# Kernel optimization log

Measured on AMD Instinct MI355X. Metric: run time of the kernel, lower is better.

Reference implementation:

```python
import jax, jax.numpy as jnp
import numpy as np

N_NODES = 50000
N_EDGES = 1600000
D_V, D_E, D_ATTN = 256, 128, 128


def setup_inputs() -> dict:
    key = jax.random.key(0)
    ks = jax.random.split(key, 10)
    scale = 0.05
    nodes = jax.random.normal(ks[0], (N_NODES, D_V), dtype=jnp.float32)
    edges = jax.random.normal(ks[1], (N_EDGES, D_E), dtype=jnp.float32)
    edge_index = jax.random.randint(ks[2], (2, N_EDGES), 0, N_NODES, dtype=jnp.int64 if jax.config.jax_enable_x64 else jnp.int32)
    Wq = jax.random.normal(ks[3], (D_ATTN, D_V), dtype=jnp.float32) * scale
    bq = jnp.zeros((D_ATTN,), dtype=jnp.float32)
    Wk = jax.random.normal(ks[4], (D_ATTN, D_V), dtype=jnp.float32) * scale
    bk = jnp.zeros((D_ATTN,), dtype=jnp.float32)
    Wv = jax.random.normal(ks[5], (D_ATTN, D_E), dtype=jnp.float32) * scale
    bv = jnp.zeros((D_ATTN,), dtype=jnp.float32)
    return {"nodes": nodes, "edges": edges, "edge_index": edge_index,
            "Wq": Wq, "bq": bq, "Wk": Wk, "bk": bk, "Wv": Wv, "bv": bv}


def reference(nodes, edges, edge_index, Wq, bq, Wk, bk, Wv, bv):
    # nodes: [N, d_v], edges: [E, d_e], edge_index: [2, E] (s=sender, r=receiver)
    s, r = edge_index[0], edge_index[1]
    lrelu = jax.nn.leaky_relu  # default negative_slope=0.01, matches torch F.leaky_relu
    q = lrelu(nodes @ Wq.T + bq)      # [N, d_attn]
    k = lrelu(nodes[s] @ Wk.T + bk)   # [E, d_attn]  (key of sender node per edge)
    v = lrelu(edges @ Wv.T + bv)      # [E, d_attn]
    d = q.shape[-1]
    # Per-edge logit = <q[r[e]], k[e]> / sqrt(d).  Masked dense softmax over the
    # [N, E] score matrix with mask (r[e]==i) is exactly a segment softmax by receiver.
    logits = jnp.sum(q[r] * k, axis=-1) / jnp.sqrt(jnp.asarray(d, q.dtype))  # [E]
    N = nodes.shape[0]
    m = jax.ops.segment_max(logits, r, num_segments=N)          # [N]
    p = jnp.exp(logits - m[r])                                  # [E]
    denom = jax.ops.segment_sum(p, r, num_segments=N)           # [N]
    attn = p / denom[r]                                         # [E]
    out = jax.ops.segment_sum(attn[:, None] * v, r, num_segments=N)  # [N, d_attn]
    return out
```

## Files before the change

### kernel.cpp

```cpp
#include <hip/hip_runtime.h>
#include <hip/hip_bf16.h>
#include <cstdint>

#define NN 50000
#define NE 1600000
#define DV 256
#define DA 128

using floatx4 = __attribute__((ext_vector_type(4))) float;
using shortx8 = __attribute__((ext_vector_type(8))) short;

__device__ __forceinline__ unsigned short f2bf(float f) {
    union { float f; uint32_t u; } v; v.f = f;
    uint32_t u = v.u;
    uint32_t r = (u + 0x7FFFu + ((u >> 16) & 1u)) >> 16;
    return (unsigned short)r;
}
__device__ __forceinline__ float bflo(uint32_t u) {
    union { uint32_t u; float f; } v; v.u = u << 16; return v.f;
}
__device__ __forceinline__ float bfhi(uint32_t u) {
    union { uint32_t u; float f; } v; v.u = u & 0xFFFF0000u; return v.f;
}

__global__ void init_zero(float4* __restrict__ out, float4* __restrict__ denom,
                          float4* __restrict__ cnt) {
    const float4 z = make_float4(0.f, 0.f, 0.f, 0.f);
    int i = blockIdx.x * blockDim.x + threadIdx.x;
    const int stride = gridDim.x * blockDim.x;
    for (int j = i; j < NN * 128 / 4; j += stride) out[j] = z;
    if (i < NN / 4) { denom[i] = z; cnt[i] = z; }
}

__global__ void cast_w_kernel(const float* __restrict__ wq, const float* __restrict__ wk,
                              const float* __restrict__ wv, unsigned short* __restrict__ out) {
    int i = blockIdx.x * blockDim.x + threadIdx.x;
    if (i < 32768)       out[i] = f2bf(wq[i]);
    else if (i < 65536)  out[i] = f2bf(wk[i - 32768]);
    else if (i < 81920)  out[i] = f2bf(wv[i - 65536]);
}

__global__ void hist_kernel(const int* __restrict__ ridx, int* __restrict__ cnt) {
    int e = blockIdx.x * blockDim.x + threadIdx.x;
    if (e < NE) atomicAdd(&cnt[ridx[e]], 1);
}

__global__ __launch_bounds__(1024)
void scan_kernel(const int* __restrict__ cnt, int* __restrict__ offs) {
    __shared__ int part[1024];
    const int tid = threadIdx.x;
    const int PER = (NN + 1023) / 1024;
    int base = tid * PER;
    int s = 0;
    for (int i = 0; i < PER; ++i) { int idx = base + i; if (idx < NN) s += cnt[idx]; }
    part[tid] = s;
    __syncthreads();
    for (int off = 1; off < 1024; off <<= 1) {
        int v = (tid >= off) ? part[tid - off] : 0;
        __syncthreads();
        part[tid] += v;
        __syncthreads();
    }
    int excl = (tid == 0) ? 0 : part[tid - 1];
    for (int i = 0; i < PER; ++i) {
        int idx = base + i;
        if (idx < NN) { offs[idx] = excl; excl += cnt[idx]; }
    }
}

__global__ void scatter_kernel(const int* __restrict__ ridx, int* __restrict__ offs,
                               int* __restrict__ perm, int* __restrict__ rs) {
    int e = blockIdx.x * blockDim.x + threadIdx.x;
    if (e >= NE) return;
    int r = ridx[e];
    int pos = atomicAdd(&offs[r], 1);
    perm[pos] = e;
    rs[pos] = r;
}

__global__ __launch_bounds__(256)
void proj_qk(const float* __restrict__ A, const unsigned short* __restrict__ Wst,
             const float* __restrict__ bq, const float* __restrict__ bk,
             unsigned short* __restrict__ qbf, unsigned short* __restrict__ kbf, int M) {
    __shared__ unsigned short Al[64 * 32];
    __shared__ unsigned short Bl[256 * 32];
    const int tid = threadIdx.x;
    const int lane = tid & 63, w = tid >> 6;
    const int m0 = blockIdx.x * 64;
    constexpr int K = 256;

    floatx4 acc[16];
#pragma unroll
    for (int i = 0; i < 16; ++i) acc[i] = (floatx4)0.0f;

    for (int kk = 0; kk < K; kk += 32) {
#pragma unroll
        for (int it = 0; it < 2; ++it) {
            int j = tid + it * 256;
            int row = j >> 3;
            int c4 = (j & 7) * 4;
            float4 f = make_float4(0.f, 0.f, 0.f, 0.f);
            int gm = m0 + row;
            if (gm < M) f = *reinterpret_cast<const float4*>(A + (size_t)gm * K + kk + c4);
            ushort4 u; u.x = f2bf(f.x); u.y = f2bf(f.y); u.z = f2bf(f.z); u.w = f2bf(f.w);
            *reinterpret_cast<ushort4*>(&Al[row * 32 + c4]) = u;
        }
#pragma unroll
        for (int it = 0; it < 4; ++it) {
            int j = tid + it * 256;
            int row = j >> 2;
            int c8 = (j & 3) * 8;
            uint4 v = *reinterpret_cast<const uint4*>(Wst + (size_t)row * K + kk + c8);
            *reinterpret_cast<uint4*>(&Bl[row * 32 + c8]) = v;
        }
        __syncthreads();
        shortx8 af = *reinterpret_cast<const shortx8*>(&Al[(w * 16 + (lane & 15)) * 32 + 8 * (lane >> 4)]);
#pragma unroll
        for (int nt = 0; nt < 16; ++nt) {
            shortx8 bf = *reinterpret_cast<const shortx8*>(&Bl[(nt * 16 + (lane & 15)) * 32 + 8 * (lane >> 4)]);
            acc[nt] = __builtin_amdgcn_mfma_f32_16x16x32_bf16(af, bf, acc[nt], 0, 0, 0);
        }
        __syncthreads();
    }
    const int col = lane & 15;
    const int rbase = m0 + w * 16 + 4 * (lane >> 4);
#pragma unroll
    for (int nt = 0; nt < 16; ++nt) {
        int gn = nt * 16 + col;
        bool isq = gn < 128;
        int oc = isq ? gn : gn - 128;
        float b = isq ? bq[oc] : bk[oc];
        unsigned short* O = isq ? qbf : kbf;
#pragma unroll
        for (int reg = 0; reg < 4; ++reg) {
            int gm = rbase + reg;
            if (gm < M) {
                float v = acc[nt][reg] + b;
                v = v > 0.f ? v : 0.01f * v;
                O[(size_t)gm * 128 + oc] = f2bf(v);
            }
        }
    }
}

__global__ __launch_bounds__(256)
void v_gemm_fused(const float* __restrict__ Ed, const unsigned short* __restrict__ Wv,
                  const float* __restrict__ bv,
                  const unsigned short* __restrict__ qbf, const unsigned short* __restrict__ kbf,
                  const int* __restrict__ sidx,
                  const int* __restrict__ perm, const int* __restrict__ rs,
                  float* __restrict__ out, float* __restrict__ denom) {
    constexpr int K = 128;
    constexpr int VLD = 129;
    __shared__ float Vl[64 * VLD];
    __shared__ float pl[64];
    __shared__ int segstart[64];
    __shared__ int segnode[64];
    __shared__ int nseg_s;
    unsigned short* Al = reinterpret_cast<unsigned short*>(Vl);
    unsigned short* Bl = reinterpret_cast<unsigned short*>(Vl) + 2048;

    const int tid = threadIdx.x;
    const int lane = tid & 63, w = tid >> 6;
    const int m0 = blockIdx.x * 64;

    if (w == 0) {
        int r = rs[m0 + lane];
        int prev = (lane == 0) ? -1 : rs[m0 + lane - 1];
        bool flag = (lane == 0) || (r != prev);
        unsigned long long mask = __ballot(flag);
        int ns = __popcll(mask);
        int pos = __popcll(mask & ((1ull << lane) - 1ull));
        if (flag) { segstart[pos] = lane; segnode[pos] = r; }
        if (lane == 0) nseg_s = ns;
    }

    {
        const int eL = tid >> 2;
        const int qt = tid & 3;
        int posE = m0 + eL;
        int e = perm[posE];
        int s = sidx[e];
        int r = rs[posE];
        const uint4* kp = reinterpret_cast<const uint4*>(kbf + (size_t)s * 128 + qt * 32);
        const uint4* qp = reinterpret_cast<const uint4*>(qbf + (size_t)r * 128 + qt * 32);
        float acc = 0.f;
#pragma unroll
        for (int i = 0; i < 4; ++i) {
            uint4 qa = qp[i], ka = kp[i];
            acc += bflo(qa.x) * bflo(ka.x) + bfhi(qa.x) * bfhi(ka.x);
            acc += bflo(qa.y) * bflo(ka.y) + bfhi(qa.y) * bfhi(ka.y);
            acc += bflo(qa.z) * bflo(ka.z) + bfhi(qa.z) * bfhi(ka.z);
            acc += bflo(qa.w) * bflo(ka.w) + bfhi(qa.w) * bfhi(ka.w);
        }
        acc += __shfl_xor(acc, 1);
        acc += __shfl_xor(acc, 2);
        if (qt == 0) pl[eL] = __expf(acc * 0.08838834764831845f);
    }

    const int row0 = tid >> 3;
    const int e0 = perm[m0 + row0];
    const int e1 = perm[m0 + row0 + 32];
    const int c4 = (tid & 7) * 4;

    floatx4 acc[8];
#pragma unroll
    for (int i = 0; i < 8; ++i) acc[i] = (floatx4)0.0f;

    for (int kk = 0; kk < K; kk += 32) {
        {
            float4 f0 = *reinterpret_cast<const float4*>(Ed + (size_t)e0 * K + kk + c4);
            float4 f1 = *reinterpret_cast<const float4*>(Ed + (size_t)e1 * K + kk + c4);
            ushort4 u0; u0.x = f2bf(f0.x); u0.y = f2bf(f0.y); u0.z = f2bf(f0.z); u0.w = f2bf(f0.w);
            ushort4 u1; u1.x = f2bf(f1.x); u1.y = f2bf(f1.y); u1.z = f2bf(f1.z); u1.w = f2bf(f1.w);
            *reinterpret_cast<ushort4*>(&Al[row0 * 32 + c4]) = u0;
            *reinterpret_cast<ushort4*>(&Al[(row0 + 32) * 32 + c4]) = u1;
        }
#pragma unroll
        for (int it = 0; it < 2; ++it) {
            int j = tid + it * 256;
            int row = j >> 2;
            int c8 = (j & 3) * 8;
            uint4 v = *reinterpret_cast<const uint4*>(Wv + (size_t)row * K + kk + c8);
            *reinterpret_cast<uint4*>(&Bl[row * 32 + c8]) = v;
        }
        __syncthreads();
        shortx8 af = *reinterpret_cast<const shortx8*>(&Al[(w * 16 + (lane & 15)) * 32 + 8 * (lane >> 4)]);
#pragma unroll
        for (int nt = 0; nt < 8; ++nt) {
            shortx8 bf = *reinterpret_cast<const shortx8*>(&Bl[(nt * 16 + (lane & 15)) * 32 + 8 * (lane >> 4)]);
            acc[nt] = __builtin_amdgcn_mfma_f32_16x16x32_bf16(af, bf, acc[nt], 0, 0, 0);
        }
        __syncthreads();
    }

    const int col = lane & 15;
    const int lrbase = w * 16 + 4 * (lane >> 4);
    float pe[4];
#pragma unroll
    for (int reg = 0; reg < 4; ++reg) pe[reg] = pl[lrbase + reg];
#pragma unroll
    for (int nt = 0; nt < 8; ++nt) {
        int gn = nt * 16 + col;
        float b = bv[gn];
#pragma unroll
        for (int reg = 0; reg < 4; ++reg) {
            float v = acc[nt][reg] + b;
            v = v > 0.f ? v : 0.01f * v;
            Vl[(lrbase + reg) * VLD + gn] = v * pe[reg];
        }
    }
    __syncthreads();

    const int colc = tid & 127;
    const int sg = tid >> 7;
    const int ns = nseg_s;
    for (int s2 = sg; s2 < ns; s2 += 2) {
        int a = segstart[s2];
        int bnd = (s2 + 1 < ns) ? segstart[s2 + 1] : 64;
        float sum = 0.f;
        for (int rr = a; rr < bnd; ++rr) sum += Vl[rr * VLD + colc];
        atomicAdd(&out[(size_t)segnode[s2] * 128 + colc], sum);
        if (colc == 0) {
            float ds = 0.f;
            for (int rr = a; rr < bnd; ++rr) ds += pl[rr];
            atomicAdd(&denom[segnode[s2]], ds);
        }
    }
}

__global__ void normalize_kernel(float* __restrict__ out, const float* __restrict__ denom) {
    int i = blockIdx.x * blockDim.x + threadIdx.x;
    if (i >= NN * 128 / 4) return;
    int node = (i * 4) >> 7;
    float d = denom[node];
    float inv = d > 0.f ? 1.0f / d : 0.f;
    float4* o = reinterpret_cast<float4*>(out) + i;
    float4 v = *o;
    v.x *= inv; v.y *= inv; v.z *= inv; v.w *= inv;
    *o = v;
}

extern "C" void kernel_launch(void* const* d_in, const int* in_sizes, int n_in,
                              void* d_out, int out_size, void* d_ws, size_t ws_size,
                              hipStream_t stream) {
    const float* nodes = (const float*)d_in[0];
    const float* edges = (const float*)d_in[1];
    const int*   eidx  = (const int*)d_in[2];
    const float* Wq = (const float*)d_in[3];
    const float* bq = (const float*)d_in[4];
    const float* Wk = (const float*)d_in[5];
    const float* bk = (const float*)d_in[6];
    const float* Wv = (const float*)d_in[7];
    const float* bv = (const float*)d_in[8];
    const int* sidx = eidx;
    const int* ridx = eidx + NE;

    char* ws = (char*)d_ws;
    unsigned short* wq_bf = (unsigned short*)ws;
    unsigned short* wv_bf = wq_bf + 65536;
    unsigned short* q_bf  = (unsigned short*)(ws + 163840);
    unsigned short* k_bf  = q_bf + (size_t)NN * 128;
    char* ws2 = ws + 163840 + 2 * (size_t)NN * 128 * 2;
    float* denom = (float*)ws2;
    int*   cnt   = (int*)(denom + NN);
    int*   offs  = cnt + NN;
    int*   perm  = offs + NN;
    int*   rs    = perm + NE;
    float* out = (float*)d_out;

    init_zero<<<2048, 256, 0, stream>>>((float4*)out, (float4*)denom, (float4*)cnt);
    cast_w_kernel<<<320, 256, 0, stream>>>(Wq, Wk, Wv, wq_bf);
    hist_kernel<<<(NE + 255) / 256, 256, 0, stream>>>(ridx, cnt);
    scan_kernel<<<1, 1024, 0, stream>>>(cnt, offs);
    scatter_kernel<<<(NE + 255) / 256, 256, 0, stream>>>(ridx, offs, perm, rs);
    proj_qk<<<(NN + 63) / 64, 256, 0, stream>>>(nodes, wq_bf, bq, bk, q_bf, k_bf, NN);
    v_gemm_fused<<<NE / 64, 256, 0, stream>>>(edges, wv_bf, bv, q_bf, k_bf, sidx, perm, rs, out, denom);
    normalize_kernel<<<(NN * 128 / 4 + 255) / 256, 256, 0, stream>>>(out, denom);
}
```

Measured before the change: 680.9 us.

## Restructure fused V-GEMM: 128-edge tiles, preloaded swizzled weights, double-buffered A, direct stores

The fused edge kernel now handles 128 edges per 512-thread block. It loads the whole bf16 Wv into shared memory once in MFMA fragment order and double-buffers the edge feature tiles with an XOR swizzle, so each k-step needs one barrier instead of two. The rs array is dropped: receivers are read through ridx via perm, and segment boundaries are found with two wavefront ballots. Segments that lie fully inside a tile are written with plain stores instead of atomics, and the staged V tile is held as bf16, which saves shared memory but adds some rounding error.

```diff
diff --git a/kernel.cpp b/kernel.cpp
--- a/kernel.cpp
+++ b/kernel.cpp
@@ -21,6 +21,14 @@
 }
 __device__ __forceinline__ float bfhi(uint32_t u) {
     union { uint32_t u; float f; } v; v.u = u & 0xFFFF0000u; return v.f;
+}
+__device__ __forceinline__ shortx8 pack8(float4 a, float4 b) {
+    shortx8 u;
+    u[0] = (short)f2bf(a.x); u[1] = (short)f2bf(a.y);
+    u[2] = (short)f2bf(a.z); u[3] = (short)f2bf(a.w);
+    u[4] = (short)f2bf(b.x); u[5] = (short)f2bf(b.y);
+    u[6] = (short)f2bf(b.z); u[7] = (short)f2bf(b.w);
+    return u;
 }
 
 __global__ void init_zero(float4* __restrict__ out, float4* __restrict__ denom,
@@ -69,13 +77,12 @@
 }
 
 __global__ void scatter_kernel(const int* __restrict__ ridx, int* __restrict__ offs,
-                               int* __restrict__ perm, int* __restrict__ rs) {
+                               int* __restrict__ perm) {
     int e = blockIdx.x * blockDim.x + threadIdx.x;
     if (e >= NE) return;
     int r = ridx[e];
     int pos = atomicAdd(&offs[r], 1);
     perm[pos] = e;
-    rs[pos] = r;
 }
 
 __global__ __launch_bounds__(256)
@@ -143,128 +150,152 @@
     }
 }
 
-__global__ __launch_bounds__(256)
-void v_gemm_fused(const float* __restrict__ Ed, const unsigned short* __restrict__ Wv,
+__global__ __launch_bounds__(512)
+void v_gemm_fused(const float* __restrict__ Ed, const unsigned short* __restrict__ wv_bf,
                   const float* __restrict__ bv,
                   const unsigned short* __restrict__ qbf, const unsigned short* __restrict__ kbf,
-                  const int* __restrict__ sidx,
-                  const int* __restrict__ perm, const int* __restrict__ rs,
+                  const int* __restrict__ sidx, const int* __restrict__ ridx,
+                  const int* __restrict__ perm,
                   float* __restrict__ out, float* __restrict__ denom) {
-    constexpr int K = 128;
-    constexpr int VLD = 129;
-    __shared__ float Vl[64 * VLD];
-    __shared__ float pl[64];
-    __shared__ int segstart[64];
-    __shared__ int segnode[64];
-    __shared__ int nseg_s;
-    unsigned short* Al = reinterpret_cast<unsigned short*>(Vl);
-    unsigned short* Bl = reinterpret_cast<unsigned short*>(Vl) + 2048;
+    __shared__ __align__(16) char smem[51264];
+    unsigned short* Bf = reinterpret_cast<unsigned short*>(smem);
+    unsigned short* Vl = reinterpret_cast<unsigned short*>(smem);
+    int*   rs_local = reinterpret_cast<int*>(smem + 49152);
+    float* pl       = reinterpret_cast<float*>(smem + 49664);
+    int*   segstart = reinterpret_cast<int*>(smem + 50176);
+    int*   segnode  = reinterpret_cast<int*>(smem + 50688);
+    unsigned long long* masks = reinterpret_cast<unsigned long long*>(smem + 51200);
+    int* nseg_s = reinterpret_cast<int*>(smem + 51216);
 
     const int tid = threadIdx.x;
     const int lane = tid & 63, w = tid >> 6;
-    const int m0 = blockIdx.x * 64;
-
-    if (w == 0) {
-        int r = rs[m0 + lane];
-        int prev = (lane == 0) ? -1 : rs[m0 + lane - 1];
-        bool flag = (lane == 0) || (r != prev);
-        unsigned long long mask = __ballot(flag);
-        int ns = __popcll(mask);
-        int pos = __popcll(mask & ((1ull << lane) - 1ull));
-        if (flag) { segstart[pos] = lane; segnode[pos] = r; }
-        if (lane == 0) nseg_s = ns;
-    }
+    const size_t m0 = (size_t)blockIdx.x * 128;
+
+    const int erow = tid >> 2;
+    const int qt = tid & 3;
+    const int e_id = perm[m0 + erow];
+    const int sN = sidx[e_id];
+    const int rN = ridx[e_id];
+    if (qt == 0) rs_local[erow] = rN;
 
     {
-        const int eL = tid >> 2;
-        const int qt = tid & 3;
-        int posE = m0 + eL;
-        int e = perm[posE];
-        int s = sidx[e];
-        int r = rs[posE];
-        const uint4* kp = reinterpret_cast<const uint4*>(kbf + (size_t)s * 128 + qt * 32);
-        const uint4* qp = reinterpret_cast<const uint4*>(qbf + (size_t)r * 128 + qt * 32);
-        float acc = 0.f;
+        const uint4* kp = reinterpret_cast<const uint4*>(kbf + (size_t)sN * 128 + qt * 32);
+        const uint4* qp = reinterpret_cast<const uint4*>(qbf + (size_t)rN * 128 + qt * 32);
+        float acq = 0.f;
 #pragma unroll
         for (int i = 0; i < 4; ++i) {
             uint4 qa = qp[i], ka = kp[i];
-            acc += bflo(qa.x) * bflo(ka.x) + bfhi(qa.x) * bfhi(ka.x);
-            acc += bflo(qa.y) * bflo(ka.y) + bfhi(qa.y) * bfhi(ka.y);
-            acc += bflo(qa.z) * bflo(ka.z) + bfhi(qa.z) * bfhi(ka.z);
-            acc += bflo(qa.w) * bflo(ka.w) + bfhi(qa.w) * bfhi(ka.w);
-        }
-        acc += __shfl_xor(acc, 1);
-        acc += __shfl_xor(acc, 2);
-        if (qt == 0) pl[eL] = __expf(acc * 0.08838834764831845f);
-    }
-
-    const int row0 = tid >> 3;
-    const int e0 = perm[m0 + row0];
-    const int e1 = perm[m0 + row0 + 32];
-    const int c4 = (tid & 7) * 4;
+            acq += bflo(qa.x) * bflo(ka.x) + bfhi(qa.x) * bfhi(ka.x);
+            acq += bflo(qa.y) * bflo(ka.y) + bfhi(qa.y) * bfhi(ka.y);
+            acq += bflo(qa.z) * bflo(ka.z) + bfhi(qa.z) * bfhi(ka.z);
+            acq += bflo(qa.w) * bflo(ka.w) + bfhi(qa.w) * bfhi(ka.w);
+        }
+        acq += __shfl_xor(acq, 1);
+        acq += __shfl_xor(acq, 2);
+        if (qt == 0) pl[erow] = __expf(acq * 0.08838834764831845f);
+    }
+
+#pragma unroll
+    for (int it = 0; it < 4; ++it) {
+        int s = tid + it * 512;
+        int g = s >> 6, l = s & 63;
+        int kt4 = g >> 3, nt = g & 7;
+        uint4 v = *reinterpret_cast<const uint4*>(
+            wv_bf + (size_t)(nt * 16 + (l & 15)) * 128 + kt4 * 32 + 8 * (l >> 4));
+        *reinterpret_cast<uint4*>(smem + s * 16) = v;
+    }
+
+    const float* arow = Ed + (size_t)e_id * 128;
+    const int cst = (tid & 3) * 8;
+    const int chunkp = (tid & 3) ^ ((tid >> 3) & 3);
+    {
+        float4 fa = *reinterpret_cast<const float4*>(arow + cst);
+        float4 fb = *reinterpret_cast<const float4*>(arow + cst + 4);
+        shortx8 u = pack8(fa, fb);
+        *reinterpret_cast<shortx8*>(smem + 32768 + erow * 64 + chunkp * 16) = u;
+    }
+    __syncthreads();
+
+    if (tid < 128) {
+        bool flag = (tid == 0) || (rs_local[tid] != rs_local[tid - 1]);
+        unsigned long long mk = __ballot(flag);
+        if (lane == 0) masks[w] = mk;
+    }
+    __syncthreads();
+    if (tid < 128) {
+        bool flag = (tid == 0) || (rs_local[tid] != rs_local[tid - 1]);
+        unsigned long long mk0 = masks[0], mk1 = masks[1];
+        if (tid == 0) *nseg_s = __popcll(mk0) + __popcll(mk1);
+        if (flag) {
+            int rank = (tid < 64)
+                ? __popcll(mk0 & ((1ull << tid) - 1ull))
+                : __popcll(mk0) + ((tid == 64) ? 0 : __popcll(mk1 & ((1ull << (tid - 64)) - 1ull)));
+            segstart[rank] = tid;
+            segnode[rank] = rs_local[tid];
+        }
+    }
 
     floatx4 acc[8];
 #pragma unroll
     for (int i = 0; i < 8; ++i) acc[i] = (floatx4)0.0f;
-
-    for (int kk = 0; kk < K; kk += 32) {
-        {
-            float4 f0 = *reinterpret_cast<const float4*>(Ed + (size_t)e0 * K + kk + c4);
-            float4 f1 = *reinterpret_cast<const float4*>(Ed + (size_t)e1 * K + kk + c4);
-            ushort4 u0; u0.x = f2bf(f0.x); u0.y = f2bf(f0.y); u0.z = f2bf(f0.z); u0.w = f2bf(f0.w);
-            ushort4 u1; u1.x = f2bf(f1.x); u1.y = f2bf(f1.y); u1.z = f2bf(f1.z); u1.w = f2bf(f1.w);
-            *reinterpret_cast<ushort4*>(&Al[row0 * 32 + c4]) = u0;
-            *reinterpret_cast<ushort4*>(&Al[(row0 + 32) * 32 + c4]) = u1;
-        }
-#pragma unroll
-        for (int it = 0; it < 2; ++it) {
-            int j = tid + it * 256;
-            int row = j >> 2;
-            int c8 = (j & 3) * 8;
-            uint4 v = *reinterpret_cast<const uint4*>(Wv + (size_t)row * K + kk + c8);
-            *reinterpret_cast<uint4*>(&Bl[row * 32 + c8]) = v;
-        }
-        __syncthreads();
-        shortx8 af = *reinterpret_cast<const shortx8*>(&Al[(w * 16 + (lane & 15)) * 32 + 8 * (lane >> 4)]);
+    const int afr_off = (w * 16 + (lane & 15)) * 64 +
+                        (((lane >> 4) ^ (((lane & 15) >> 1) & 3)) << 4);
+#pragma unroll
+    for (int kt = 0; kt < 4; ++kt) {
+        const int rbase = (kt & 1) ? 40960 : 32768;
+        const int wbase = (kt & 1) ? 32768 : 40960;
+        float4 fa, fb;
+        if (kt < 3) {
+            fa = *reinterpret_cast<const float4*>(arow + (kt + 1) * 32 + cst);
+            fb = *reinterpret_cast<const float4*>(arow + (kt + 1) * 32 + cst + 4);
+        }
+        shortx8 af = *reinterpret_cast<const shortx8*>(smem + rbase + afr_off);
 #pragma unroll
         for (int nt = 0; nt < 8; ++nt) {
-            shortx8 bf = *reinterpret_cast<const shortx8*>(&Bl[(nt * 16 + (lane & 15)) * 32 + 8 * (lane >> 4)]);
-            acc[nt] = __builtin_amdgcn_mfma_f32_16x16x32_bf16(af, bf, acc[nt], 0, 0, 0);
-        }
-        __syncthreads();
-    }
-
-    const int col = lane & 15;
-    const int lrbase = w * 16 + 4 * (lane >> 4);
+            shortx8 bfr = *reinterpret_cast<const shortx8*>(smem + (((kt * 8 + nt) * 64 + lane) << 4));
+            acc[nt] = __builtin_amdgcn_mfma_f32_16x16x32_bf16(af, bfr, acc[nt], 0, 0, 0);
+        }
+        if (kt < 3) {
+            shortx8 u = pack8(fa, fb);
+            *reinterpret_cast<shortx8*>(smem + wbase + erow * 64 + chunkp * 16) = u;
+        }
+        __syncthreads();
+    }
+
+    const int colb = lane & 15;
+    const int rquad = w * 16 + 4 * (lane >> 4);
     float pe[4];
 #pragma unroll
-    for (int reg = 0; reg < 4; ++reg) pe[reg] = pl[lrbase + reg];
+    for (int reg = 0; reg < 4; ++reg) pe[reg] = pl[rquad + reg];
 #pragma unroll
     for (int nt = 0; nt < 8; ++nt) {
-        int gn = nt * 16 + col;
-        float b = bv[gn];
+        float b = bv[nt * 16 + colb];
 #pragma unroll
         for (int reg = 0; reg < 4; ++reg) {
             float v = acc[nt][reg] + b;
             v = v > 0.f ? v : 0.01f * v;
-            Vl[(lrbase + reg) * VLD + gn] = v * pe[reg];
+            Vl[(rquad + reg) * 128 + nt * 16 + colb] = f2bf(v * pe[reg]);
         }
     }
     __syncthreads();
 
     const int colc = tid & 127;
     const int sg = tid >> 7;
-    const int ns = nseg_s;
-    for (int s2 = sg; s2 < ns; s2 += 2) {
+    const int ns = *nseg_s;
+    for (int s2 = sg; s2 < ns; s2 += 4) {
         int a = segstart[s2];
-        int bnd = (s2 + 1 < ns) ? segstart[s2 + 1] : 64;
+        int bnd = (s2 + 1 < ns) ? segstart[s2 + 1] : 128;
         float sum = 0.f;
-        for (int rr = a; rr < bnd; ++rr) sum += Vl[rr * VLD + colc];
-        atomicAdd(&out[(size_t)segnode[s2] * 128 + colc], sum);
+        for (int rr = a; rr < bnd; ++rr) sum += bflo((uint32_t)Vl[rr * 128 + colc]);
+        int node = segnode[s2];
+        bool interior = (s2 > 0) && (s2 + 1 < ns);
+        if (interior) out[(size_t)node * 128 + colc] = sum;
+        else          atomicAdd(&out[(size_t)node * 128 + colc], sum);
         if (colc == 0) {
             float ds = 0.f;
             for (int rr = a; rr < bnd; ++rr) ds += pl[rr];
-            atomicAdd(&denom[segnode[s2]], ds);
+            if (interior) denom[node] = ds;
+            else          atomicAdd(&denom[node], ds);
         }
     }
 }
@@ -306,15 +337,15 @@
     int*   cnt   = (int*)(denom + NN);
     int*   offs  = cnt + NN;
     int*   perm  = offs + NN;
-    int*   rs    = perm + NE;
     float* out = (float*)d_out;
 
     init_zero<<<2048, 256, 0, stream>>>((float4*)out, (float4*)denom, (float4*)cnt);
     cast_w_kernel<<<320, 256, 0, stream>>>(Wq, Wk, Wv, wq_bf);
     hist_kernel<<<(NE + 255) / 256, 256, 0, stream>>>(ridx, cnt);
     scan_kernel<<<1, 1024, 0, stream>>>(cnt, offs);
-    scatter_kernel<<<(NE + 255) / 256, 256, 0, stream>>>(ridx, offs, perm, rs);
+    scatter_kernel<<<(NE + 255) / 256, 256, 0, stream>>>(ridx, offs, perm);
     proj_qk<<<(NN + 63) / 64, 256, 0, stream>>>(nodes, wq_bf, bq, bk, q_bf, k_bf, NN);
-    v_gemm_fused<<<NE / 64, 256, 0, stream>>>(edges, wv_bf, bv, q_bf, k_bf, sidx, perm, rs, out, denom);
+    v_gemm_fused<<<NE / 128, 512, 0, stream>>>(edges, wv_bf, bv, q_bf, k_bf, sidx, ridx,
+                                               perm, out, denom);
     normalize_kernel<<<(NN * 128 / 4 + 255) / 256, 256, 0, stream>>>(out, denom);
 }
```

After: 640.2 us. 1.06x faster.
